# Performance work log

Hardware: AMD Instinct MI355X
Metric: run time of the kernel (lower is better)

The kernel has to match this reference:

```python
import jax, jax.numpy as jnp
import numpy as np

B, S, D = 1, 4096, 768
H = 12
HD = D // H  # 64


def setup_inputs() -> dict:
    key = jax.random.key(0)
    ks = jax.random.split(key, 6)
    sc = 1.0 / np.sqrt(D)
    return {
        "x": jax.random.normal(ks[0], (B, S, D), dtype=jnp.float32),
        "wq": jax.random.normal(ks[1], (D, D), dtype=jnp.float32) * sc,
        "wk": jax.random.normal(ks[2], (D, D), dtype=jnp.float32) * sc,
        "wv": jax.random.normal(ks[3], (D, D), dtype=jnp.float32) * sc,
        "wo": jax.random.normal(ks[4], (D, D), dtype=jnp.float32) * sc,
        "bo": jax.random.normal(ks[5], (D,), dtype=jnp.float32) * 0.02,
    }


def reference(x, wq, wk, wv, wo, bo):
    b, n, _ = x.shape
    # projections (torch Linear: x @ W.T; here weights stored as (d_in, d_out))
    q = (x @ wq).reshape(b, n, H, HD).transpose(0, 2, 1, 3)  # b h n d
    k = (x @ wk).reshape(b, n, H, HD).transpose(0, 2, 1, 3)
    v = (x @ wv).reshape(b, n, H, HD).transpose(0, 2, 1, 3)
    scores = jnp.einsum("bhqd,bhkd->bhqk", q, k)
    causal = jnp.tril(jnp.ones((n, n), dtype=bool))  # True = keep
    scores = jnp.where(causal, scores, -jnp.inf)
    weights = jax.nn.softmax(scores / np.sqrt(HD), axis=-1)
    ctx = jnp.einsum("bhqk,bhkd->bhqd", weights, v)
    ctx = ctx.transpose(0, 2, 1, 3).reshape(b, n, D)
    return ctx @ wo + bo
```

## Files before the change

kernel.cpp:

```cpp
#include <hip/hip_runtime.h>


typedef short bf16x8 __attribute__((ext_vector_type(8)));
typedef float f32x4 __attribute__((ext_vector_type(4)));
typedef unsigned short u16;

static constexpr int S_LEN = 4096;
static constexpr int DIM   = 768;
static constexpr int NH    = 12;
static constexpr float QSCALE = 0.125f * 1.44269504088896340736f;

__device__ inline u16 f2bf(float f) {
  union { float f; unsigned int u; } v; v.f = f;
  unsigned int r = v.u + 0x7FFFu + ((v.u >> 16) & 1u);
  return (u16)(r >> 16);
}

__device__ inline void gload_lds16(const u16* g, u16* s) {
  __builtin_amdgcn_global_load_lds(
      (const __attribute__((address_space(1))) unsigned int*)g,
      (__attribute__((address_space(3))) unsigned int*)s, 16, 0, 0);
}

__global__ __launch_bounds__(256)
void prep_kernel(const float* __restrict__ x, const float* __restrict__ w0,
                 const float* __restrict__ w1, const float* __restrict__ w2,
                 const float* __restrict__ w3, u16* __restrict__ xb,
                 u16* __restrict__ t0, u16* __restrict__ t1,
                 u16* __restrict__ t2, u16* __restrict__ t3) {
  if (blockIdx.z == 4) {
    const size_t n = (size_t)S_LEN * DIM;
    const int id = blockIdx.y * 12 + blockIdx.x;
    const size_t stride = (size_t)144 * 256 * 8;
    for (size_t i = ((size_t)id * 256 + threadIdx.x) * 8; i < n; i += stride) {
      const float4 a = *(const float4*)(x + i);
      const float4 b = *(const float4*)(x + i + 4);
      bf16x8 o;
      o[0] = (short)f2bf(a.x); o[1] = (short)f2bf(a.y);
      o[2] = (short)f2bf(a.z); o[3] = (short)f2bf(a.w);
      o[4] = (short)f2bf(b.x); o[5] = (short)f2bf(b.y);
      o[6] = (short)f2bf(b.z); o[7] = (short)f2bf(b.w);
      *(bf16x8*)(xb + i) = o;
    }
    return;
  }
  __shared__ float T[64][65];
  const float* src; u16* dst;
  switch (blockIdx.z) {
    case 0: src = w0; dst = t0; break;
    case 1: src = w1; dst = t1; break;
    case 2: src = w2; dst = t2; break;
    default: src = w3; dst = t3; break;
  }
  const int k0 = blockIdx.y * 64, n0 = blockIdx.x * 64;
  const int r = threadIdx.x >> 2, c0 = (threadIdx.x & 3) * 16;
#pragma unroll
  for (int i = 0; i < 4; ++i) {
    const float4 v = *(const float4*)(src + (size_t)(k0 + r) * DIM + n0 + c0 + i * 4);
    T[r][c0 + i * 4 + 0] = v.x;
    T[r][c0 + i * 4 + 1] = v.y;
    T[r][c0 + i * 4 + 2] = v.z;
    T[r][c0 + i * 4 + 3] = v.w;
  }
  __syncthreads();
  bf16x8 o0, o1;
#pragma unroll
  for (int i = 0; i < 8; ++i) {
    o0[i] = (short)f2bf(T[c0 + i][r]);
    o1[i] = (short)f2bf(T[c0 + 8 + i][r]);
  }
  *(bf16x8*)(dst + (size_t)(n0 + r) * DIM + k0 + c0) = o0;
  *(bf16x8*)(dst + (size_t)(n0 + r) * DIM + k0 + c0 + 8) = o1;
}

template <int MODE>
__global__ __launch_bounds__(256)
void mfma_gemm_kernel(const u16* __restrict__ A, const u16* __restrict__ Bq,
                      const u16* __restrict__ Bk, const u16* __restrict__ Bv,
                      const float* __restrict__ bias, u16* __restrict__ Qb,
                      u16* __restrict__ Kb, u16* __restrict__ VT,
                      float* __restrict__ Out) {
  constexpr int MT = (MODE == 0) ? 4 : 2;
  constexpr int BM = MT * 32;
  __shared__ __align__(16) u16 Al[BM * 64];
  __shared__ __align__(16) u16 Bl[96 * 64];

  const int tid  = threadIdx.x;
  const int wv   = tid >> 6;
  const int lane = tid & 63;
  const int quad = lane >> 4;
  const int l16  = lane & 15;
  const int wr = wv >> 1, wc = wv & 1;
  const int m0 = blockIdx.y * BM;
  const int n0 = blockIdx.x * 96;

  int wi = 0, nb = n0;
  const u16* BT = Bq;
  if (MODE == 0) {
    wi = n0 / DIM;
    nb = n0 - wi * DIM;
    BT = (wi == 0) ? Bq : (wi == 1) ? Bk : Bv;
  }

  const int sr8 = lane >> 3;
  const int sc  = ((lane & 7) ^ sr8) * 8;
  const int key = l16 & 7;

  const bool swp = (MODE == 1) || (wi < 2);

  f32x4 acc[MT][3] = {};

  for (int k0 = 0; k0 < DIM; k0 += 64) {
    __syncthreads();
#pragma unroll
    for (int j = 0; j < MT; ++j)
      gload_lds16(A + (size_t)(m0 + wv * (BM / 4) + j * 8 + sr8) * DIM + k0 + sc,
                  &Al[(wv * (BM / 4) + j * 8) * 64]);
#pragma unroll
    for (int j = 0; j < 3; ++j)
      gload_lds16(BT + (size_t)(nb + wv * 24 + j * 8 + sr8) * DIM + k0 + sc,
                  &Bl[(wv * 24 + j * 8) * 64]);
    __syncthreads();

#pragma unroll
    for (int kh = 0; kh < 2; ++kh) {
      const int cb = kh * 4;
      bf16x8 af[MT], bfr[3];
#pragma unroll
      for (int mt = 0; mt < MT; ++mt) {
        const int row = wr * (BM / 2) + mt * 16 + l16;
        af[mt] = *(const bf16x8*)&Al[row * 64 + ((cb + quad) ^ key) * 8];
      }
#pragma unroll
      for (int nt = 0; nt < 3; ++nt) {
        const int row = wc * 48 + nt * 16 + l16;
        bfr[nt] = *(const bf16x8*)&Bl[row * 64 + ((cb + quad) ^ key) * 8];
      }
      if (swp) {
#pragma unroll
        for (int mt = 0; mt < MT; ++mt)
#pragma unroll
          for (int nt = 0; nt < 3; ++nt)
            acc[mt][nt] = __builtin_amdgcn_mfma_f32_16x16x32_bf16(
                bfr[nt], af[mt], acc[mt][nt], 0, 0, 0);
      } else {
#pragma unroll
        for (int mt = 0; mt < MT; ++mt)
#pragma unroll
          for (int nt = 0; nt < 3; ++nt)
            acc[mt][nt] = __builtin_amdgcn_mfma_f32_16x16x32_bf16(
                af[mt], bfr[nt], acc[mt][nt], 0, 0, 0);
      }
    }
  }

  if (MODE == 0 && wi >= 2) {
#pragma unroll
    for (int mt = 0; mt < MT; ++mt) {
#pragma unroll
      for (int nt = 0; nt < 3; ++nt) {
        const int row  = m0 + wr * (BM / 2) + mt * 16 + quad * 4;
        const int ncol = nb + wc * 48 + nt * 16 + l16;
        u16 pk[4];
#pragma unroll
        for (int r = 0; r < 4; ++r) pk[r] = f2bf(acc[mt][nt][r]);
        unsigned long long v;
        __builtin_memcpy(&v, pk, 8);
        *(unsigned long long*)(VT + (size_t)ncol * S_LEN + row) = v;
      }
    }
  } else if (MODE == 0) {
    u16* dst = (wi == 0) ? Qb : Kb;
    const float sc_out = (wi == 0) ? QSCALE : 1.0f;
#pragma unroll
    for (int mt = 0; mt < MT; ++mt) {
#pragma unroll
      for (int nt = 0; nt < 3; ++nt) {
        const int row = m0 + wr * (BM / 2) + mt * 16 + l16;
        const int ncb = nb + wc * 48 + nt * 16 + quad * 4;
        u16 pk[4];
#pragma unroll
        for (int r = 0; r < 4; ++r) pk[r] = f2bf(acc[mt][nt][r] * sc_out);
        unsigned long long v;
        __builtin_memcpy(&v, pk, 8);
        *(unsigned long long*)(dst + (size_t)row * DIM + ncb) = v;
      }
    }
  } else {
#pragma unroll
    for (int mt = 0; mt < MT; ++mt) {
#pragma unroll
      for (int nt = 0; nt < 3; ++nt) {
        const int row = m0 + wr * (BM / 2) + mt * 16 + l16;
        const int ncb = n0 + wc * 48 + nt * 16 + quad * 4;
        const float4 b4 = *(const float4*)(bias + ncb);
        float4 ov;
        ov.x = acc[mt][nt][0] + b4.x;
        ov.y = acc[mt][nt][1] + b4.y;
        ov.z = acc[mt][nt][2] + b4.z;
        ov.w = acc[mt][nt][3] + b4.w;
        *(float4*)(Out + (size_t)row * DIM + ncb) = ov;
      }
    }
  }
}

__global__ __launch_bounds__(256, 5)
void attn_mfma_kernel(const u16* __restrict__ Qb, const u16* __restrict__ Kb,
                      const u16* __restrict__ VTb, u16* __restrict__ ctx) {
  __shared__ __align__(16) u16 KVl[128 * 64 + 64 * 128];
  u16* const Kl = KVl;
  u16* const Vl = KVl + 128 * 64;

  const int tid  = threadIdx.x;
  const int w    = tid >> 6;
  const int lane = tid & 63;
  const int quad = lane >> 4;
  const int l16  = lane & 15;
  const int qw   = w >> 1;
  const int kw   = w & 1;
  const int key  = l16 & 7;

  const int id = blockIdx.x;
  const int to = id / 12;
  const int h  = id - to * 12;
  const int qt = 127 - to;
  const int q0 = qt * 32;

  const int sr8  = lane >> 3;
  const int scK  = ((lane & 7) ^ sr8) * 8;
  const int sr16 = lane >> 4;

  const u16* qptr = Qb + (size_t)(q0 + qw * 16 + l16) * DIM + h * 64 + quad * 8;
  const bf16x8 aq0 = *(const bf16x8*)(qptr);
  const bf16x8 aq1 = *(const bf16x8*)(qptr + 32);

  f32x4 o[4] = {};
  float l_s = 0.f;
  const int qg = q0 + qw * 16 + l16;

  const int nkt = qt / 2 + 1;
  const int niter = (nkt + 1) >> 1;
  const int my_last = nkt - 1;

#pragma unroll 1
  for (int i = 0; i < niter; ++i) {
    const int k0g = i * 128;
    asm volatile("s_waitcnt lgkmcnt(0)" ::: "memory");
    __builtin_amdgcn_s_barrier();

#pragma unroll
    for (int j = 0; j < 4; ++j)
      gload_lds16(Kb + (size_t)(k0g + w * 32 + j * 8 + sr8) * DIM + h * 64 + scK,
                  &Kl[(w * 32 + j * 8) * 64]);
#pragma unroll
    for (int j = 0; j < 4; ++j) {
      const int vrow = w * 16 + j * 4 + sr16;
      const int vcol = ((lane & 15) ^ (vrow & 7)) * 8;
      gload_lds16(VTb + (size_t)(h * 64 + vrow) * S_LEN + k0g + vcol,
                  &Vl[(w * 16 + j * 4) * 128]);
    }
    asm volatile("s_waitcnt vmcnt(4)" ::: "memory");
    __builtin_amdgcn_s_barrier();

    const int kt_w = 2 * i + kw;
    const bool act = kt_w < nkt;
    bf16x8 pa0, pa1;
    if (act) {
      __builtin_amdgcn_s_setprio(1);
      f32x4 s[4];
#pragma unroll
      for (int t = 0; t < 4; ++t) {
        const int row = kw * 64 + t * 16 + l16;
        const bf16x8 bk0 = *(const bf16x8*)&Kl[row * 64 + (quad ^ key) * 8];
        const bf16x8 bk1 = *(const bf16x8*)&Kl[row * 64 + ((quad ^ 4) ^ key) * 8];
        s[t] = __builtin_amdgcn_mfma_f32_16x16x32_bf16(
            bk0, aq0, f32x4{0.f, 0.f, 0.f, 0.f}, 0, 0, 0);
        s[t] = __builtin_amdgcn_mfma_f32_16x16x32_bf16(bk1, aq1, s[t], 0, 0, 0);
      }

      unsigned Wt[4][2];
      if (kt_w == my_last) {
#pragma unroll
        for (int t = 0; t < 4; ++t) {
          float pr[4];
#pragma unroll
          for (int r = 0; r < 4; ++r) {
            const int kvg = k0g + kw * 64 + t * 16 + quad * 4 + r;
            float p = __builtin_amdgcn_exp2f(s[t][r]);
            if (kvg > qg) p = 0.f;
            l_s += p;
            pr[r] = p;
          }
          asm("v_cvt_pk_bf16_f32 %0, %1, %2" : "=v"(Wt[t][0]) : "v"(pr[0]), "v"(pr[1]));
          asm("v_cvt_pk_bf16_f32 %0, %1, %2" : "=v"(Wt[t][1]) : "v"(pr[2]), "v"(pr[3]));
        }
      } else {
#pragma unroll
        for (int t = 0; t < 4; ++t) {
          float pr[4];
#pragma unroll
          for (int r = 0; r < 4; ++r) {
            const float p = __builtin_amdgcn_exp2f(s[t][r]);
            l_s += p;
            pr[r] = p;
          }
          asm("v_cvt_pk_bf16_f32 %0, %1, %2" : "=v"(Wt[t][0]) : "v"(pr[0]), "v"(pr[1]));
          asm("v_cvt_pk_bf16_f32 %0, %1, %2" : "=v"(Wt[t][1]) : "v"(pr[2]), "v"(pr[3]));
        }
      }

      {
        unsigned a0 = Wt[0][0], b0 = Wt[1][0];
        unsigned a1 = Wt[0][1], b1 = Wt[1][1];
        asm("v_permlane32_swap_b32 %0, %1" : "+v"(a0), "+v"(b0));
        asm("v_permlane16_swap_b32 %0, %1" : "+v"(a0), "+v"(b0));
        asm("v_permlane32_swap_b32 %0, %1" : "+v"(a1), "+v"(b1));
        asm("v_permlane16_swap_b32 %0, %1" : "+v"(a1), "+v"(b1));
        union { unsigned u[4]; bf16x8 v; } U0;
        U0.u[0] = a0; U0.u[1] = a1; U0.u[2] = b0; U0.u[3] = b1;
        pa0 = U0.v;
        unsigned c0 = Wt[2][0], d0 = Wt[3][0];
        unsigned c1 = Wt[2][1], d1 = Wt[3][1];
        asm("v_permlane32_swap_b32 %0, %1" : "+v"(c0), "+v"(d0));
        asm("v_permlane16_swap_b32 %0, %1" : "+v"(c0), "+v"(d0));
        asm("v_permlane32_swap_b32 %0, %1" : "+v"(c1), "+v"(d1));
        asm("v_permlane16_swap_b32 %0, %1" : "+v"(c1), "+v"(d1));
        union { unsigned u[4]; bf16x8 v; } U1;
        U1.u[0] = c0; U1.u[1] = c1; U1.u[2] = d0; U1.u[3] = d1;
        pa1 = U1.v;
      }
    }

    asm volatile("s_waitcnt vmcnt(0)" ::: "memory");
    __builtin_amdgcn_s_barrier();

    if (act) {
#pragma unroll
      for (int t = 0; t < 4; ++t) {
        const int row = t * 16 + l16;
        const int cc0 = (kw * 8 + quad) ^ key;
        const int cc1 = (kw * 8 + quad + 4) ^ key;
        const bf16x8 vb0 = *(const bf16x8*)&Vl[row * 128 + cc0 * 8];
        const bf16x8 vb1 = *(const bf16x8*)&Vl[row * 128 + cc1 * 8];
        o[t] = __builtin_amdgcn_mfma_f32_16x16x32_bf16(pa0, vb0, o[t], 0, 0, 0);
        o[t] = __builtin_amdgcn_mfma_f32_16x16x32_bf16(pa1, vb1, o[t], 0, 0, 0);
      }
      __builtin_amdgcn_s_setprio(0);
    }
  }

  __syncthreads();
  float* Obuf  = (float*)KVl;
  float* lbufF = Obuf + 5120;
#pragma unroll
  for (int t = 0; t < 4; ++t)
    *(f32x4*)&Obuf[(w * 64 + lane) * 20 + t * 4] = o[t];
  lbufF[w * 64 + lane] = l_s;
  __syncthreads();
#pragma unroll
  for (int t = 0; t < 4; ++t) {
    const f32x4 po = *(const f32x4*)&Obuf[((w ^ 1) * 64 + lane) * 20 + t * 4];
    o[t] += po;
  }
  l_s += lbufF[(w ^ 1) * 64 + lane];

  if (kw == 0) {
    float L = l_s;
    L += __shfl_xor(L, 16);
    L += __shfl_xor(L, 32);
#pragma unroll
    for (int r = 0; r < 4; ++r) {
      const float inv = 1.f / __shfl(L, quad * 4 + r);
      const int row = q0 + qw * 16 + quad * 4 + r;
#pragma unroll
      for (int t = 0; t < 4; ++t)
        ctx[(size_t)row * DIM + h * 64 + t * 16 + l16] = f2bf(o[t][r] * inv);
    }
  }
}

extern "C" void kernel_launch(void* const* d_in, const int* in_sizes, int n_in,
                              void* d_out, int out_size, void* d_ws,
                              size_t ws_size, hipStream_t stream) {
  const float* x  = (const float*)d_in[0];
  const float* wq = (const float*)d_in[1];
  const float* wk = (const float*)d_in[2];
  const float* wv = (const float*)d_in[3];
  const float* wo = (const float*)d_in[4];
  const float* bo = (const float*)d_in[5];

  const size_t n_x = (size_t)S_LEN * DIM;
  const size_t n_w = (size_t)DIM * DIM;
  u16* xb  = (u16*)d_ws;
  u16* wtq = xb + n_x;
  u16* wtk = wtq + n_w;
  u16* wtv = wtk + n_w;
  u16* wto = wtv + n_w;
  u16* Qb  = wto + n_w;
  u16* Kb  = Qb + n_x;
  u16* VTb = Kb + n_x;
  u16* ctx = VTb + n_x;

  prep_kernel<<<dim3(12, 12, 5), 256, 0, stream>>>(
      x, wq, wk, wv, wo, xb, wtq, wtk, wtv, wto);

  mfma_gemm_kernel<0><<<dim3(24, 32), 256, 0, stream>>>(
      xb, wtq, wtk, wtv, nullptr, Qb, Kb, VTb, nullptr);

  attn_mfma_kernel<<<dim3(1536), 256, 0, stream>>>(Qb, Kb, VTb, ctx);

  mfma_gemm_kernel<1><<<dim3(8, 64), 256, 0, stream>>>(
      ctx, wto, nullptr, nullptr, bo, nullptr, nullptr, nullptr, (float*)d_out);
}
```

Measured before the change: 154.9 us.

## Split attention KV range into chunks with separate combine kernel

Splits each query tile's causal key range into up to four chunks of 8 iterations, launching 4x more attention blocks that write unnormalized partial outputs and row sums to a float workspace. A new combine kernel sums the partials, normalizes and writes bf16 context. The aim is to fix load imbalance and the long tail from the causal triangle, where the longest query tiles serialize many KV iterations. In exchange it adds a kernel launch, extra global traffic for the partials, and many blocks that exit early. The partials can be summed directly only because the softmax uses no running max.

```diff
diff --git a/kernel.cpp b/kernel.cpp
--- a/kernel.cpp
+++ b/kernel.cpp
@@ -207,7 +207,7 @@
 
 __global__ __launch_bounds__(256, 5)
 void attn_mfma_kernel(const u16* __restrict__ Qb, const u16* __restrict__ Kb,
-                      const u16* __restrict__ VTb, u16* __restrict__ ctx) {
+                      const u16* __restrict__ VTb, float* __restrict__ pbuf) {
   __shared__ __align__(16) u16 KVl[128 * 64 + 64 * 128];
   u16* const Kl = KVl;
   u16* const Vl = KVl + 128 * 64;
@@ -222,10 +222,20 @@
   const int key  = l16 & 7;
 
   const int id = blockIdx.x;
-  const int to = id / 12;
-  const int h  = id - to * 12;
+  const int h  = id % 12;
+  const int j  = id / 12;
+  const int ck = j & 3;
+  const int to = j >> 2;
   const int qt = 127 - to;
   const int q0 = qt * 32;
+
+  const int nkt = qt / 2 + 1;
+  const int niter = (nkt + 1) >> 1;
+  const int my_last = nkt - 1;
+
+  const int i0 = ck * 8;
+  if (i0 >= niter) return;
+  const int i1 = (i0 + 8 < niter) ? (i0 + 8) : niter;
 
   const int sr8  = lane >> 3;
   const int scK  = ((lane & 7) ^ sr8) * 8;
@@ -239,26 +249,22 @@
   float l_s = 0.f;
   const int qg = q0 + qw * 16 + l16;
 
-  const int nkt = qt / 2 + 1;
-  const int niter = (nkt + 1) >> 1;
-  const int my_last = nkt - 1;
-
 #pragma unroll 1
-  for (int i = 0; i < niter; ++i) {
+  for (int i = i0; i < i1; ++i) {
     const int k0g = i * 128;
     asm volatile("s_waitcnt lgkmcnt(0)" ::: "memory");
     __builtin_amdgcn_s_barrier();
 
 #pragma unroll
-    for (int j = 0; j < 4; ++j)
-      gload_lds16(Kb + (size_t)(k0g + w * 32 + j * 8 + sr8) * DIM + h * 64 + scK,
-                  &Kl[(w * 32 + j * 8) * 64]);
-#pragma unroll
-    for (int j = 0; j < 4; ++j) {
-      const int vrow = w * 16 + j * 4 + sr16;
+    for (int jj = 0; jj < 4; ++jj)
+      gload_lds16(Kb + (size_t)(k0g + w * 32 + jj * 8 + sr8) * DIM + h * 64 + scK,
+                  &Kl[(w * 32 + jj * 8) * 64]);
+#pragma unroll
+    for (int jj = 0; jj < 4; ++jj) {
+      const int vrow = w * 16 + jj * 4 + sr16;
       const int vcol = ((lane & 15) ^ (vrow & 7)) * 8;
       gload_lds16(VTb + (size_t)(h * 64 + vrow) * S_LEN + k0g + vcol,
-                  &Vl[(w * 16 + j * 4) * 128]);
+                  &Vl[(w * 16 + jj * 4) * 128]);
     }
     asm volatile("s_waitcnt vmcnt(4)" ::: "memory");
     __builtin_amdgcn_s_barrier();
@@ -369,15 +375,46 @@
     float L = l_s;
     L += __shfl_xor(L, 16);
     L += __shfl_xor(L, 32);
+    float* pe = pbuf + ((size_t)(to * 4 + ck) * 12 + h) * 2080;
+    if (quad == 0) pe[2048 + qw * 16 + l16] = L;
 #pragma unroll
     for (int r = 0; r < 4; ++r) {
-      const float inv = 1.f / __shfl(L, quad * 4 + r);
-      const int row = q0 + qw * 16 + quad * 4 + r;
+      const int row = qw * 16 + quad * 4 + r;
 #pragma unroll
       for (int t = 0; t < 4; ++t)
-        ctx[(size_t)row * DIM + h * 64 + t * 16 + l16] = f2bf(o[t][r] * inv);
-    }
-  }
+        pe[row * 64 + t * 16 + l16] = o[t][r];
+    }
+  }
+}
+
+__global__ __launch_bounds__(256)
+void attn_combine(const float* __restrict__ pbuf, u16* __restrict__ ctx) {
+  const int id = blockIdx.x;
+  const int h  = id % 12;
+  const int to = id / 12;
+  const int qt = 127 - to;
+  const int niter = (qt / 2 + 2) >> 1;
+  const int nch = (niter + 7) >> 3;
+
+  const int row = threadIdx.x >> 3;
+  const int dc  = (threadIdx.x & 7) * 8;
+
+  f32x4 a0 = {}, a1 = {};
+  float lsum = 0.f;
+  for (int c = 0; c < nch; ++c) {
+    const float* pe = pbuf + ((size_t)(to * 4 + c) * 12 + h) * 2080;
+    a0 += *(const f32x4*)(pe + row * 64 + dc);
+    a1 += *(const f32x4*)(pe + row * 64 + dc + 4);
+    lsum += pe[2048 + row];
+  }
+  const float inv = 1.f / lsum;
+  bf16x8 ov;
+#pragma unroll
+  for (int jj = 0; jj < 4; ++jj) {
+    ov[jj]     = (short)f2bf(a0[jj] * inv);
+    ov[jj + 4] = (short)f2bf(a1[jj] * inv);
+  }
+  *(bf16x8*)(ctx + (size_t)(qt * 32 + row) * DIM + h * 64 + dc) = ov;
 }
 
 extern "C" void kernel_launch(void* const* d_in, const int* in_sizes, int n_in,
@@ -401,6 +438,7 @@
   u16* Kb  = Qb + n_x;
   u16* VTb = Kb + n_x;
   u16* ctx = VTb + n_x;
+  float* pbuf = (float*)(ctx + n_x);
 
   prep_kernel<<<dim3(12, 12, 5), 256, 0, stream>>>(
       x, wq, wk, wv, wo, xb, wtq, wtk, wtv, wto);
@@ -408,7 +446,9 @@
   mfma_gemm_kernel<0><<<dim3(24, 32), 256, 0, stream>>>(
       xb, wtq, wtk, wtv, nullptr, Qb, Kb, VTb, nullptr);
 
-  attn_mfma_kernel<<<dim3(1536), 256, 0, stream>>>(Qb, Kb, VTb, ctx);
+  attn_mfma_kernel<<<dim3(6144), 256, 0, stream>>>(Qb, Kb, VTb, pbuf);
+
+  attn_combine<<<dim3(1536), 256, 0, stream>>>(pbuf, ctx);
 
   mfma_gemm_kernel<1><<<dim3(8, 64), 256, 0, stream>>>(
       ctx, wto, nullptr, nullptr, bo, nullptr, nullptr, nullptr, (float*)d_out);
```

After: 170.6 us. 1.1x slower.

## Read V directly from global memory instead of staging through LDS

Applied to the files above, without the earlier changes.

The V^T tile is no longer copied into shared memory. Each wave loads its V operands for the PV MFMAs straight from global memory, which removes the second barrier and waitcnt per iteration. LDS use shrinks to the K tile plus the epilogue reduction buffer, and launch bounds rise to allow 7 blocks per CU for higher occupancy. The cost is uncoalesced, uncached-in-LDS global loads of V sitting on the critical path just before the MFMAs, and the K load now waits with vmcnt(0) instead of overlapping the V load.

```diff
diff --git a/kernel.cpp b/kernel.cpp
--- a/kernel.cpp
+++ b/kernel.cpp
@@ -205,12 +205,11 @@
   }
 }
 
-__global__ __launch_bounds__(256, 5)
+__global__ __launch_bounds__(256, 7)
 void attn_mfma_kernel(const u16* __restrict__ Qb, const u16* __restrict__ Kb,
                       const u16* __restrict__ VTb, u16* __restrict__ ctx) {
-  __shared__ __align__(16) u16 KVl[128 * 64 + 64 * 128];
-  u16* const Kl = KVl;
-  u16* const Vl = KVl + 128 * 64;
+  __shared__ __align__(16) u16 Sm[10752];
+  u16* const Kl = Sm;
 
   const int tid  = threadIdx.x;
   const int w    = tid >> 6;
@@ -229,7 +228,6 @@
 
   const int sr8  = lane >> 3;
   const int scK  = ((lane & 7) ^ sr8) * 8;
-  const int sr16 = lane >> 4;
 
   const u16* qptr = Qb + (size_t)(q0 + qw * 16 + l16) * DIM + h * 64 + quad * 8;
   const bf16x8 aq0 = *(const bf16x8*)(qptr);
@@ -253,20 +251,11 @@
     for (int j = 0; j < 4; ++j)
       gload_lds16(Kb + (size_t)(k0g + w * 32 + j * 8 + sr8) * DIM + h * 64 + scK,
                   &Kl[(w * 32 + j * 8) * 64]);
-#pragma unroll
-    for (int j = 0; j < 4; ++j) {
-      const int vrow = w * 16 + j * 4 + sr16;
-      const int vcol = ((lane & 15) ^ (vrow & 7)) * 8;
-      gload_lds16(VTb + (size_t)(h * 64 + vrow) * S_LEN + k0g + vcol,
-                  &Vl[(w * 16 + j * 4) * 128]);
-    }
-    asm volatile("s_waitcnt vmcnt(4)" ::: "memory");
+    asm volatile("s_waitcnt vmcnt(0)" ::: "memory");
     __builtin_amdgcn_s_barrier();
 
     const int kt_w = 2 * i + kw;
-    const bool act = kt_w < nkt;
-    bf16x8 pa0, pa1;
-    if (act) {
+    if (kt_w < nkt) {
       __builtin_amdgcn_s_setprio(1);
       f32x4 s[4];
 #pragma unroll
@@ -310,6 +299,7 @@
         }
       }
 
+      bf16x8 pa0, pa1;
       {
         unsigned a0 = Wt[0][0], b0 = Wt[1][0];
         unsigned a1 = Wt[0][1], b1 = Wt[1][1];
@@ -330,19 +320,13 @@
         U1.u[0] = c0; U1.u[1] = c1; U1.u[2] = d0; U1.u[3] = d1;
         pa1 = U1.v;
       }
-    }
-
-    asm volatile("s_waitcnt vmcnt(0)" ::: "memory");
-    __builtin_amdgcn_s_barrier();
-
-    if (act) {
+
 #pragma unroll
       for (int t = 0; t < 4; ++t) {
-        const int row = t * 16 + l16;
-        const int cc0 = (kw * 8 + quad) ^ key;
-        const int cc1 = (kw * 8 + quad + 4) ^ key;
-        const bf16x8 vb0 = *(const bf16x8*)&Vl[row * 128 + cc0 * 8];
-        const bf16x8 vb1 = *(const bf16x8*)&Vl[row * 128 + cc1 * 8];
+        const u16* vp = VTb + (size_t)(h * 64 + t * 16 + l16) * S_LEN
+                        + k0g + kw * 64 + quad * 8;
+        const bf16x8 vb0 = *(const bf16x8*)(vp);
+        const bf16x8 vb1 = *(const bf16x8*)(vp + 32);
         o[t] = __builtin_amdgcn_mfma_f32_16x16x32_bf16(pa0, vb0, o[t], 0, 0, 0);
         o[t] = __builtin_amdgcn_mfma_f32_16x16x32_bf16(pa1, vb1, o[t], 0, 0, 0);
       }
@@ -351,7 +335,7 @@
   }
 
   __syncthreads();
-  float* Obuf  = (float*)KVl;
+  float* Obuf  = (float*)Sm;
   float* lbufF = Obuf + 5120;
 #pragma unroll
   for (int t = 0; t < 4; ++t)
```

Measured after the change: 246.4 us. 1.59x slower.

## Split attention KV tiles across four warps, each covering both query sets

Applied to the files above, without the earlier changes.

Each of the four warps now takes a 32-key slice of the 128-key tile and handles both 16-row query sets, where before two warps split queries and two split keys. Every K and V fragment read from LDS now feeds two query sets, so fewer LDS reads are issued per MFMA and causal work is spread across warps at 32-key granularity. The cost is a larger cross-warp reduction at the end: a butterfly over four warps with extra barriers, and more accumulator registers per warp (two sets of o), which may lower occupancy.

```diff
diff --git a/kernel.cpp b/kernel.cpp
--- a/kernel.cpp
+++ b/kernel.cpp
@@ -217,8 +217,6 @@
   const int lane = tid & 63;
   const int quad = lane >> 4;
   const int l16  = lane & 15;
-  const int qw   = w >> 1;
-  const int kw   = w & 1;
   const int key  = l16 & 7;
 
   const int id = blockIdx.x;
@@ -231,17 +229,19 @@
   const int scK  = ((lane & 7) ^ sr8) * 8;
   const int sr16 = lane >> 4;
 
-  const u16* qptr = Qb + (size_t)(q0 + qw * 16 + l16) * DIM + h * 64 + quad * 8;
-  const bf16x8 aq0 = *(const bf16x8*)(qptr);
-  const bf16x8 aq1 = *(const bf16x8*)(qptr + 32);
-
-  f32x4 o[4] = {};
-  float l_s = 0.f;
-  const int qg = q0 + qw * 16 + l16;
-
-  const int nkt = qt / 2 + 1;
-  const int niter = (nkt + 1) >> 1;
-  const int my_last = nkt - 1;
+  bf16x8 aq[2][2];
+#pragma unroll
+  for (int set = 0; set < 2; ++set) {
+    const u16* qp = Qb + (size_t)(q0 + set * 16 + l16) * DIM + h * 64 + quad * 8;
+    aq[set][0] = *(const bf16x8*)(qp);
+    aq[set][1] = *(const bf16x8*)(qp + 32);
+  }
+
+  f32x4 o[2][4] = {};
+  float l_s[2] = {0.f, 0.f};
+  const int qg[2] = {q0 + l16, q0 + 16 + l16};
+
+  const int niter = qt / 4 + 1;
 
 #pragma unroll 1
   for (int i = 0; i < niter; ++i) {
@@ -250,85 +250,81 @@
     __builtin_amdgcn_s_barrier();
 
 #pragma unroll
-    for (int j = 0; j < 4; ++j)
-      gload_lds16(Kb + (size_t)(k0g + w * 32 + j * 8 + sr8) * DIM + h * 64 + scK,
-                  &Kl[(w * 32 + j * 8) * 64]);
-#pragma unroll
-    for (int j = 0; j < 4; ++j) {
-      const int vrow = w * 16 + j * 4 + sr16;
-      const int vcol = ((lane & 15) ^ (vrow & 7)) * 8;
+    for (int jj = 0; jj < 4; ++jj)
+      gload_lds16(Kb + (size_t)(k0g + w * 32 + jj * 8 + sr8) * DIM + h * 64 + scK,
+                  &Kl[(w * 32 + jj * 8) * 64]);
+#pragma unroll
+    for (int jj = 0; jj < 4; ++jj) {
+      const int vrow = w * 16 + jj * 4 + sr16;
+      const int vcol = (l16 ^ (vrow & 7)) * 8;
       gload_lds16(VTb + (size_t)(h * 64 + vrow) * S_LEN + k0g + vcol,
-                  &Vl[(w * 16 + j * 4) * 128]);
+                  &Vl[(w * 16 + jj * 4) * 128]);
     }
     asm volatile("s_waitcnt vmcnt(4)" ::: "memory");
     __builtin_amdgcn_s_barrier();
 
-    const int kt_w = 2 * i + kw;
-    const bool act = kt_w < nkt;
-    bf16x8 pa0, pa1;
+    const int g = 4 * i + w;
+    const bool act = g <= qt;
+    bf16x8 pa[2];
     if (act) {
       __builtin_amdgcn_s_setprio(1);
-      f32x4 s[4];
-#pragma unroll
-      for (int t = 0; t < 4; ++t) {
-        const int row = kw * 64 + t * 16 + l16;
-        const bf16x8 bk0 = *(const bf16x8*)&Kl[row * 64 + (quad ^ key) * 8];
-        const bf16x8 bk1 = *(const bf16x8*)&Kl[row * 64 + ((quad ^ 4) ^ key) * 8];
-        s[t] = __builtin_amdgcn_mfma_f32_16x16x32_bf16(
-            bk0, aq0, f32x4{0.f, 0.f, 0.f, 0.f}, 0, 0, 0);
-        s[t] = __builtin_amdgcn_mfma_f32_16x16x32_bf16(bk1, aq1, s[t], 0, 0, 0);
-      }
-
-      unsigned Wt[4][2];
-      if (kt_w == my_last) {
-#pragma unroll
-        for (int t = 0; t < 4; ++t) {
-          float pr[4];
-#pragma unroll
-          for (int r = 0; r < 4; ++r) {
-            const int kvg = k0g + kw * 64 + t * 16 + quad * 4 + r;
-            float p = __builtin_amdgcn_exp2f(s[t][r]);
-            if (kvg > qg) p = 0.f;
-            l_s += p;
-            pr[r] = p;
+      const bool diag = (g == qt);
+      bf16x8 bk[2][2];
+#pragma unroll
+      for (int t = 0; t < 2; ++t) {
+        const int row = w * 32 + t * 16 + l16;
+        bk[t][0] = *(const bf16x8*)&Kl[row * 64 + (quad ^ key) * 8];
+        bk[t][1] = *(const bf16x8*)&Kl[row * 64 + ((quad ^ 4) ^ key) * 8];
+      }
+#pragma unroll
+      for (int set = 0; set < 2; ++set) {
+        f32x4 s[2];
+#pragma unroll
+        for (int t = 0; t < 2; ++t) {
+          s[t] = __builtin_amdgcn_mfma_f32_16x16x32_bf16(
+              bk[t][0], aq[set][0], f32x4{0.f, 0.f, 0.f, 0.f}, 0, 0, 0);
+          s[t] = __builtin_amdgcn_mfma_f32_16x16x32_bf16(
+              bk[t][1], aq[set][1], s[t], 0, 0, 0);
+        }
+        unsigned Wt[2][2];
+        if (diag) {
+#pragma unroll
+          for (int t = 0; t < 2; ++t) {
+            float pr[4];
+#pragma unroll
+            for (int r = 0; r < 4; ++r) {
+              const int kvg = k0g + w * 32 + t * 16 + quad * 4 + r;
+              float p = __builtin_amdgcn_exp2f(s[t][r]);
+              if (kvg > qg[set]) p = 0.f;
+              l_s[set] += p;
+              pr[r] = p;
+            }
+            asm("v_cvt_pk_bf16_f32 %0, %1, %2" : "=v"(Wt[t][0]) : "v"(pr[0]), "v"(pr[1]));
+            asm("v_cvt_pk_bf16_f32 %0, %1, %2" : "=v"(Wt[t][1]) : "v"(pr[2]), "v"(pr[3]));
           }
-          asm("v_cvt_pk_bf16_f32 %0, %1, %2" : "=v"(Wt[t][0]) : "v"(pr[0]), "v"(pr[1]));
-          asm("v_cvt_pk_bf16_f32 %0, %1, %2" : "=v"(Wt[t][1]) : "v"(pr[2]), "v"(pr[3]));
+        } else {
+#pragma unroll
+          for (int t = 0; t < 2; ++t) {
+            float pr[4];
+#pragma unroll
+            for (int r = 0; r < 4; ++r) {
+              const float p = __builtin_amdgcn_exp2f(s[t][r]);
+              l_s[set] += p;
+              pr[r] = p;
+            }
+            asm("v_cvt_pk_bf16_f32 %0, %1, %2" : "=v"(Wt[t][0]) : "v"(pr[0]), "v"(pr[1]));
+            asm("v_cvt_pk_bf16_f32 %0, %1, %2" : "=v"(Wt[t][1]) : "v"(pr[2]), "v"(pr[3]));
+          }
         }
-      } else {
-#pragma unroll
-        for (int t = 0; t < 4; ++t) {
-          float pr[4];
-#pragma unroll
-          for (int r = 0; r < 4; ++r) {
-            const float p = __builtin_amdgcn_exp2f(s[t][r]);
-            l_s += p;
-            pr[r] = p;
-          }
-          asm("v_cvt_pk_bf16_f32 %0, %1, %2" : "=v"(Wt[t][0]) : "v"(pr[0]), "v"(pr[1]));
-          asm("v_cvt_pk_bf16_f32 %0, %1, %2" : "=v"(Wt[t][1]) : "v"(pr[2]), "v"(pr[3]));
-        }
-      }
-
-      {
         unsigned a0 = Wt[0][0], b0 = Wt[1][0];
         unsigned a1 = Wt[0][1], b1 = Wt[1][1];
         asm("v_permlane32_swap_b32 %0, %1" : "+v"(a0), "+v"(b0));
         asm("v_permlane16_swap_b32 %0, %1" : "+v"(a0), "+v"(b0));
         asm("v_permlane32_swap_b32 %0, %1" : "+v"(a1), "+v"(b1));
         asm("v_permlane16_swap_b32 %0, %1" : "+v"(a1), "+v"(b1));
-        union { unsigned u[4]; bf16x8 v; } U0;
-        U0.u[0] = a0; U0.u[1] = a1; U0.u[2] = b0; U0.u[3] = b1;
-        pa0 = U0.v;
-        unsigned c0 = Wt[2][0], d0 = Wt[3][0];
-        unsigned c1 = Wt[2][1], d1 = Wt[3][1];
-        asm("v_permlane32_swap_b32 %0, %1" : "+v"(c0), "+v"(d0));
-        asm("v_permlane16_swap_b32 %0, %1" : "+v"(c0), "+v"(d0));
-        asm("v_permlane32_swap_b32 %0, %1" : "+v"(c1), "+v"(d1));
-        asm("v_permlane16_swap_b32 %0, %1" : "+v"(c1), "+v"(d1));
-        union { unsigned u[4]; bf16x8 v; } U1;
-        U1.u[0] = c0; U1.u[1] = c1; U1.u[2] = d0; U1.u[3] = d1;
-        pa1 = U1.v;
+        union { unsigned u[4]; bf16x8 v; } U;
+        U.u[0] = a0; U.u[1] = a1; U.u[2] = b0; U.u[3] = b1;
+        pa[set] = U.v;
       }
     }
 
@@ -336,15 +332,12 @@
     __builtin_amdgcn_s_barrier();
 
     if (act) {
+      const int cc = ((w * 4 + quad) ^ key);
 #pragma unroll
       for (int t = 0; t < 4; ++t) {
-        const int row = t * 16 + l16;
-        const int cc0 = (kw * 8 + quad) ^ key;
-        const int cc1 = (kw * 8 + quad + 4) ^ key;
-        const bf16x8 vb0 = *(const bf16x8*)&Vl[row * 128 + cc0 * 8];
-        const bf16x8 vb1 = *(const bf16x8*)&Vl[row * 128 + cc1 * 8];
-        o[t] = __builtin_amdgcn_mfma_f32_16x16x32_bf16(pa0, vb0, o[t], 0, 0, 0);
-        o[t] = __builtin_amdgcn_mfma_f32_16x16x32_bf16(pa1, vb1, o[t], 0, 0, 0);
+        const bf16x8 vb = *(const bf16x8*)&Vl[(t * 16 + l16) * 128 + cc * 8];
+        o[0][t] = __builtin_amdgcn_mfma_f32_16x16x32_bf16(pa[0], vb, o[0][t], 0, 0, 0);
+        o[1][t] = __builtin_amdgcn_mfma_f32_16x16x32_bf16(pa[1], vb, o[1][t], 0, 0, 0);
       }
       __builtin_amdgcn_s_setprio(0);
     }
@@ -354,28 +347,34 @@
   float* Obuf  = (float*)KVl;
   float* lbufF = Obuf + 5120;
 #pragma unroll
-  for (int t = 0; t < 4; ++t)
-    *(f32x4*)&Obuf[(w * 64 + lane) * 20 + t * 4] = o[t];
-  lbufF[w * 64 + lane] = l_s;
-  __syncthreads();
-#pragma unroll
-  for (int t = 0; t < 4; ++t) {
-    const f32x4 po = *(const f32x4*)&Obuf[((w ^ 1) * 64 + lane) * 20 + t * 4];
-    o[t] += po;
-  }
-  l_s += lbufF[(w ^ 1) * 64 + lane];
-
-  if (kw == 0) {
-    float L = l_s;
+  for (int r = 1; r <= 2; ++r) {
+#pragma unroll
+    for (int set = 0; set < 2; ++set) {
+#pragma unroll
+      for (int t = 0; t < 4; ++t)
+        *(f32x4*)&Obuf[(w * 64 + lane) * 20 + t * 4] = o[set][t];
+      lbufF[w * 64 + lane] = l_s[set];
+      __syncthreads();
+#pragma unroll
+      for (int t = 0; t < 4; ++t)
+        o[set][t] += *(const f32x4*)&Obuf[((w ^ r) * 64 + lane) * 20 + t * 4];
+      l_s[set] += lbufF[(w ^ r) * 64 + lane];
+      __syncthreads();
+    }
+  }
+
+  if (w < 2) {
+    const int set = w;
+    float L = l_s[set];
     L += __shfl_xor(L, 16);
     L += __shfl_xor(L, 32);
 #pragma unroll
     for (int r = 0; r < 4; ++r) {
       const float inv = 1.f / __shfl(L, quad * 4 + r);
-      const int row = q0 + qw * 16 + quad * 4 + r;
+      const int row = q0 + set * 16 + quad * 4 + r;
 #pragma unroll
       for (int t = 0; t < 4; ++t)
-        ctx[(size_t)row * DIM + h * 64 + t * 16 + l16] = f2bf(o[t][r] * inv);
+        ctx[(size_t)row * DIM + h * 64 + t * 16 + l16] = f2bf(o[set][t][r] * inv);
     }
   }
 }
```

After: 254.0 us. 64.0% more time.
